# Optimization experiments

Measured on AMD Instinct MI355X. Metric: run time of the kernel, lower is better.

Reference implementation:

```python
import jax, jax.numpy as jnp
import numpy as np

N_QUBITS = 12
LAYERS = 4
ENCODERS = ['angle_rx', 'angle_ry', 'h_angle_rx', 'h_angle_ry']

_INV_SQRT2 = 1.0 / np.sqrt(2.0)
H_GATE = jnp.array([[_INV_SQRT2, _INV_SQRT2], [_INV_SQRT2, -_INV_SQRT2]], dtype=jnp.complex64)


def rx_mat(t):
    # t: scalar or (B,) -> (...,2,2)
    c = jnp.cos(t / 2).astype(jnp.complex64)
    s = jnp.sin(t / 2).astype(jnp.complex64)
    return jnp.stack([jnp.stack([c, -1j * s], -1), jnp.stack([-1j * s, c], -1)], -2)


def ry_mat(t):
    c = jnp.cos(t / 2).astype(jnp.complex64)
    s = jnp.sin(t / 2).astype(jnp.complex64)
    return jnp.stack([jnp.stack([c, -s], -1), jnp.stack([s, c], -1)], -2)


def rz_mat(t):
    e = jnp.exp(-1j * t.astype(jnp.complex64) / 2)
    z = jnp.zeros_like(e)
    return jnp.stack([jnp.stack([e, z], -1), jnp.stack([z, jnp.conj(e)], -1)], -2)


def apply_1q(state, U, q, n):
    # state: (B, 2^n); wire q is axis q in big-endian (PennyLane) ordering
    B = state.shape[0]
    L, R = 2 ** q, 2 ** (n - q - 1)
    s = state.reshape(B, L, 2, R)
    if U.ndim == 2:
        s = jnp.einsum('ab,BLbR->BLaR', U, s)
    else:  # per-sample gate (B,2,2)
        s = jnp.einsum('Bab,BLbR->BLaR', U, s)
    return s.reshape(B, 2 ** n)


def apply_cnot_adjacent(state, q, n):
    # CNOT(control=q, target=q+1)
    B = state.shape[0]
    L, R = 2 ** q, 2 ** (n - q - 2)
    s = state.reshape(B, L, 2, 2, R)
    s = jnp.stack([s[:, :, 0], s[:, :, 1, ::-1]], axis=2)
    return s.reshape(B, 2 ** n)


def run_circuit(features, theta, encoder, n, layers):
    B = features.shape[0]
    state = jnp.zeros((B, 2 ** n), dtype=jnp.complex64).at[:, 0].set(1.0)
    use_h = encoder.startswith('h_')
    rot = rx_mat if encoder.endswith('rx') else ry_mat
    # encoding: one angle per qubit, batched gate
    for q in range(n):
        if use_h:
            state = apply_1q(state, H_GATE, q, n)
        state = apply_1q(state, rot(features[:, q]), q, n)
    # variational block (hadamard=False)
    for l in range(layers):
        for q in range(n):
            state = apply_1q(state, rx_mat(theta[l, q, 0]), q, n)
            state = apply_1q(state, ry_mat(theta[l, q, 1]), q, n)
            state = apply_1q(state, rz_mat(theta[l, q, 2]), q, n)
        for q in range(0, n - 1, 2):
            state = apply_cnot_adjacent(state, q, n)
        for q in range(1, n - 1, 2):
            state = apply_cnot_adjacent(state, q, n)
    # <Z_q> for every qubit
    p = jnp.abs(state) ** 2  # (B, 2^n)
    ez = []
    for q in range(n):
        pr = p.reshape(B, 2 ** q, 2, -1)
        ez.append(pr[:, :, 0].sum((1, 2)) - pr[:, :, 1].sum((1, 2)))
    return jnp.stack(ez, axis=-1)  # (B, n)


def setup_inputs() -> dict:
    key = jax.random.key(0)
    k1, k2 = jax.random.split(key)
    features = jax.random.uniform(k1, (1024, N_QUBITS), dtype=jnp.float32)
    theta = 0.01 * jax.random.normal(k2, (LAYERS, N_QUBITS, 3), dtype=jnp.float32)
    alpha = jnp.zeros((len(ENCODERS),), dtype=jnp.float32)
    return {"features": features, "theta": theta, "alpha": alpha}


def reference(features, theta, alpha):
    arch_w = jax.nn.softmax(alpha)
    branch = jnp.stack(
        [run_circuit(features, theta, enc, N_QUBITS, LAYERS) for enc in ENCODERS], axis=0
    )  # (E, B, n_qubits)
    y = jnp.einsum('e,ebq->bq', arch_w, branch)
    return y
```

## Files before the change

kernel.cpp:

```cpp
#include <hip/hip_runtime.h>
#include <math.h>

#define NQ 12
#define DIM 4096
#define NL 4
#define THREADS 256
#define SWZC(e) ((e) ^ (((e) >> 3) & 14) ^ (((e) >> 7) & 15))
#define WAVEFENCE() { __builtin_amdgcn_wave_barrier(); __builtin_amdgcn_sched_barrier(0); }

typedef float v2f __attribute__((ext_vector_type(2)));

__device__ __forceinline__ v2f pkfma(v2f a, v2f b, v2f c) {
    v2f d; asm("v_pk_fma_f32 %0, %1, %2, %3" : "=v"(d) : "v"(a), "v"(b), "v"(c)); return d;
}
__device__ __forceinline__ v2f pkmul(v2f a, v2f b) {
    v2f d; asm("v_pk_mul_f32 %0, %1, %2" : "=v"(d) : "v"(a), "v"(b)); return d;
}
__device__ __forceinline__ v2f pkadd(v2f a, v2f b) {
    v2f d; asm("v_pk_add_f32 %0, %1, %2" : "=v"(d) : "v"(a), "v"(b)); return d;
}
__device__ __forceinline__ float2 cmulS(float2 a, float2 b) {
    return make_float2(fmaf(a.x, b.x, -a.y * b.y), fmaf(a.x, b.y, a.y * b.x));
}

struct C4 { v2f r, i, ni, nr; };

#define CMUL4(orE, orI, KR, KNI, KI, xre, xim) \
    { orE = pkfma(KNI, xim, pkmul(KR, xre)); orI = pkfma(KI, xre, pkmul(KR, xim)); }
#define CMAC4(orE, orI, KR, KNI, KI, xre, xim) \
    { orE = pkfma(KR, xre, pkfma(KNI, xim, orE)); orI = pkfma(KR, xim, pkfma(KI, xre, orI)); }

#define QUADBODY(A_, B_, C_, D_) { \
    v2f z0r,z0i,z1r,z1i,z2r,z2i,z3r,z3i; \
    CMUL4(z0r,z0i, la.r, la.ni, la.i, sre[A_], sim[A_]); CMAC4(z0r,z0i, lb.r, lb.ni, lb.i, sre[B_], sim[B_]); \
    CMUL4(z1r,z1i, lb.nr, lb.ni, lb.i, sre[A_], sim[A_]); CMAC4(z1r,z1i, la.r, la.i, la.ni, sre[B_], sim[B_]); \
    CMUL4(z2r,z2i, la.r, la.ni, la.i, sre[C_], sim[C_]); CMAC4(z2r,z2i, lb.r, lb.ni, lb.i, sre[D_], sim[D_]); \
    CMUL4(z3r,z3i, lb.nr, lb.ni, lb.i, sre[C_], sim[C_]); CMAC4(z3r,z3i, la.r, la.i, la.ni, sre[D_], sim[D_]); \
    v2f y0r,y0i,y1r,y1i,y2r,y2i,y3r,y3i; \
    CMUL4(y0r,y0i, ha.r, ha.ni, ha.i, z0r, z0i); CMAC4(y0r,y0i, hb.r, hb.ni, hb.i, z2r, z2i); \
    CMUL4(y1r,y1i, ha.r, ha.ni, ha.i, z1r, z1i); CMAC4(y1r,y1i, hb.r, hb.ni, hb.i, z3r, z3i); \
    CMUL4(y2r,y2i, hb.nr, hb.ni, hb.i, z0r, z0i); CMAC4(y2r,y2i, ha.r, ha.i, ha.ni, z2r, z2i); \
    CMUL4(y3r,y3i, hb.nr, hb.ni, hb.i, z1r, z1i); CMAC4(y3r,y3i, ha.r, ha.i, ha.ni, z3r, z3i); \
    sre[A_]=y0r; sim[A_]=y0i; sre[B_]=y1r; sim[B_]=y1i; \
    sre[C_]=y3r; sim[C_]=y3i; sre[D_]=y2r; sim[D_]=y2i; }

__device__ __forceinline__ void pass_hi(v2f* sre, v2f* sim, const v2f (*U)[4]) {
    C4 la={U[0][0],U[0][1],U[0][2],U[0][3]}, lb={U[1][0],U[1][1],U[1][2],U[1][3]},
       ha={U[2][0],U[2][1],U[2][2],U[2][3]}, hb={U[3][0],U[3][1],U[3][2],U[3][3]};
    QUADBODY(0,4,8,12) QUADBODY(1,5,9,13) QUADBODY(2,6,10,14) QUADBODY(3,7,11,15)
}
__device__ __forceinline__ void pass_lo(v2f* sre, v2f* sim, const v2f (*U)[4]) {
    C4 la={U[0][0],U[0][1],U[0][2],U[0][3]}, lb={U[1][0],U[1][1],U[1][2],U[1][3]},
       ha={U[2][0],U[2][1],U[2][2],U[2][3]}, hb={U[3][0],U[3][1],U[3][2],U[3][3]};
    QUADBODY(0,1,2,3) QUADBODY(4,5,6,7) QUADBODY(8,9,10,11) QUADBODY(12,13,14,15)
}

__global__ __launch_bounds__(THREADS, 2)
void vqc_kernel(const float* __restrict__ features,
                const float* __restrict__ theta,
                const float* __restrict__ alpha,
                float* __restrict__ out)
{
    __shared__ v2f scrR[DIM];
    __shared__ v2f scrI[DIM];
    __shared__ v2f Upk[24][4][4];
    __shared__ v2f red[12 * 4];
    __shared__ float wez[12];

    float2* cs = (float2*)scrR;
    float2 (*U48)[4] = (float2(*)[4])((char*)scrR + 1152);
    float2 (*enc)[2] = (float2(*)[2])((char*)scrR + 2688);
    float2 (*pairT)[4] = (float2(*)[4])((char*)scrR + 3072);
    float2* loc = (float2*)((char*)scrR + 3456);

    const int tid = threadIdx.x;
    const bool special = (blockIdx.x == 0);
    const int gA = special ? 0 : 2 * ((int)blockIdx.x - 1);
    const int gB = gA + 1;

    if (tid < NL * NQ * 3) {
        float s, c; sincosf(0.5f * theta[tid], &s, &c);
        cs[tid] = make_float2(c, s);
    }
    if (tid >= 160 && tid < 184) {
        int c_ = (tid - 160) / 12, q = (tid - 160) % 12;
        const float r_ = 0.70710678118654752f;
        float2 a0, a1;
        if (special) { a0 = make_float2(r_, 0.f); a1 = a0; }
        else {
            int g = c_ ? gB : gA;
            int esl = g % 3, b = g / 3;
            float f = features[b * NQ + q];
            float s, c; sincosf(0.5f * f, &s, &c);
            if (esl == 0)      { a0 = make_float2(c, 0.f); a1 = make_float2(0.f, -s); }
            else if (esl == 1) { a0 = make_float2(c, 0.f); a1 = make_float2(s, 0.f); }
            else               { a0 = make_float2((c-s)*r_, 0.f); a1 = make_float2((c+s)*r_, 0.f); }
        }
        enc[c_ * NQ + q][0] = a0; enc[c_ * NQ + q][1] = a1;
    }
    __syncthreads();

    if (tid < NL * NQ) {
        float c0 = cs[tid*3+0].x, s0 = cs[tid*3+0].y;
        float c1 = cs[tid*3+1].x, s1 = cs[tid*3+1].y;
        float c2 = cs[tid*3+2].x, s2 = cs[tid*3+2].y;
        float2 a00 = make_float2( c1*c0,  s1*s0);
        float2 a01 = make_float2(-s1*c0, -c1*s0);
        float2 a10 = make_float2( s1*c0, -c1*s0);
        float2 a11 = make_float2( c1*c0, -s1*s0);
        float2 ep = make_float2(c2, -s2), em = make_float2(c2, s2);
        U48[tid][0] = cmulS(ep, a00); U48[tid][1] = cmulS(ep, a01);
        U48[tid][2] = cmulS(em, a10); U48[tid][3] = cmulS(em, a11);
    }
    if (tid >= 64 && tid < 112) {
        int x = tid - 64;
        int c_ = x / 24, y = x % 24, p = y >> 2, v = y & 3;
        pairT[c_ * 6 + p][v] = cmulS(enc[c_*NQ + 2*p][v >> 1], enc[c_*NQ + 2*p + 1][v & 1]);
    }
    __syncthreads();

    for (int idx = tid; idx < 384; idx += THREADS) {
        int p = idx >> 4, rest = idx & 15, c = rest >> 2, comp = rest & 3;
        int l = p / 6, m = p % 6;
        int q = (c < 2) ? (2*m + 1) : (2*m);
        float2 u = U48[l*NQ + q][c & 1];
        float xv = (comp == 0) ? u.x : (comp == 1) ? u.y : (comp == 2) ? -u.y : -u.x;
        v2f vv = {xv, xv};
        Upk[p][c][comp] = vv;
    }
    if (tid >= 192 && tid < 224) {
        int x = tid - 192; int c_ = x >> 4, j = x & 15;
        loc[c_ * 16 + j] = cmulS(pairT[c_*6 + 4][j >> 2], pairT[c_*6 + 5][j & 3]);
    }
    __syncthreads();

    v2f sre[16], sim[16];
    {
        int t = tid;
        float2 preA = cmulS(cmulS(pairT[0][(t>>6)&3], pairT[1][(t>>4)&3]),
                            cmulS(pairT[2][(t>>2)&3], pairT[3][t&3]));
        float2 preB = cmulS(cmulS(pairT[6][(t>>6)&3], pairT[7][(t>>4)&3]),
                            cmulS(pairT[8][(t>>2)&3], pairT[9][t&3]));
        #pragma unroll
        for (int j = 0; j < 16; ++j) {
            float2 aA = cmulS(preA, loc[j]);
            float2 aB = cmulS(preB, loc[16 + j]);
            v2f r = {aA.x, aB.x}, ii = {aA.y, aB.y};
            sre[j] = r; sim[j] = ii;
        }
    }
    __syncthreads();

    const int ba = SWZC(tid << 4);
    const int bb = SWZC((((tid >> 4) << 8) | (tid & 15)));
    const int bc = SWZC(tid);
    const int sx = (tid << 4) ^ ((tid & 1) << 3) ^ (((tid >> 2) & 1) << 5)
                             ^ (((tid >> 4) & 1) << 7) ^ (((tid >> 6) & 1) << 9);
    const int bs = SWZC(sx);

    #pragma unroll 1
    for (int l = 0; l < NL; ++l) {
        if (l > 0) {
            #pragma unroll
            for (int j = 0; j < 16; ++j) {
                int a = bs ^ (j ^ ((j >> 1) & 2));
                sre[j] = scrR[a]; sim[j] = scrI[a];
            }
        }
        pass_hi(sre, sim, Upk[l*6 + 4]);
        pass_lo(sre, sim, Upk[l*6 + 5]);
        WAVEFENCE();
        #pragma unroll
        for (int j = 0; j < 16; ++j) { int a = ba ^ j; scrR[a] = sre[j]; scrI[a] = sim[j]; }
        WAVEFENCE();
        #pragma unroll
        for (int j = 0; j < 16; ++j) { int a = bb ^ SWZC(j << 4); sre[j] = scrR[a]; sim[j] = scrI[a]; }
        pass_hi(sre, sim, Upk[l*6 + 2]);
        pass_lo(sre, sim, Upk[l*6 + 3]);
        WAVEFENCE();
        #pragma unroll
        for (int j = 0; j < 16; ++j) { int a = bb ^ SWZC(j << 4); scrR[a] = sre[j]; scrI[a] = sim[j]; }
        __syncthreads();
        #pragma unroll
        for (int j = 0; j < 16; ++j) { int a = bc ^ SWZC(j << 8); sre[j] = scrR[a]; sim[j] = scrI[a]; }
        pass_hi(sre, sim, Upk[l*6 + 0]);
        if (l < NL - 1) __syncthreads();
        pass_lo(sre, sim, Upk[l*6 + 1]);
        if (l < NL - 1) {
            #pragma unroll
            for (int j = 0; j < 16; ++j) { int a = bc ^ SWZC(j << 8); scrR[a] = sre[j]; scrI[a] = sim[j]; }
            __syncthreads();
        }
    }

    v2f s0 = {0.f,0.f}, s1 = {0.f,0.f}, s2 = {0.f,0.f}, s3 = {0.f,0.f}, psum = {0.f,0.f};
    {
        const v2f MONE = {-1.f, -1.f};
        #pragma unroll
        for (int j = 0; j < 16; ++j) {
            v2f p = pkfma(sim[j], sim[j], pkmul(sre[j], sre[j]));
            psum = pkadd(psum, p);
            if (j & 8)                        s0 = pkfma(p, MONE, s0); else s0 = pkadd(s0, p);
            if (j & 4)                        s1 = pkfma(p, MONE, s1); else s1 = pkadd(s1, p);
            if ((((j >> 1) ^ (j >> 2)) & 1))  s2 = pkfma(p, MONE, s2); else s2 = pkadd(s2, p);
            if (j & 1)                        s3 = pkfma(p, MONE, s3); else s3 = pkadd(s3, p);
        }
    }
    v2f vals[12];
    {
        int t = tid;
        int mt = t ^ ((t >> 1) & 0xAA);
        vals[0] = s0; vals[1] = s1; vals[2] = s2; vals[3] = s3;
        vals[4]  = ((t >> 7) & 1)  ? -s3 : s3;
        vals[5]  = ((mt >> 6) & 1) ? -psum : psum;
        vals[6]  = ((mt >> 5) & 1) ? -psum : psum;
        vals[7]  = ((mt >> 4) & 1) ? -psum : psum;
        vals[8]  = ((mt >> 3) & 1) ? -psum : psum;
        vals[9]  = ((mt >> 2) & 1) ? -psum : psum;
        vals[10] = ((mt >> 1) & 1) ? -psum : psum;
        vals[11] = (mt & 1)        ? -psum : psum;
    }
    const int lane = tid & 63, wv = tid >> 6;
    #pragma unroll
    for (int q = 0; q < 12; ++q) {
        v2f v = vals[q];
        #pragma unroll
        for (int mm = 32; mm >= 1; mm >>= 1) {
            v.x += __shfl_xor(v.x, mm, 64);
            v.y += __shfl_xor(v.y, mm, 64);
        }
        if (lane == 0) red[q * 4 + wv] = v;
    }
    __syncthreads();

    if (tid < 12) {
        v2f v = pkadd(pkadd(red[tid*4+0], red[tid*4+1]), pkadd(red[tid*4+2], red[tid*4+3]));
        float A0 = alpha[0], A1 = alpha[1], A2 = alpha[2], A3 = alpha[3];
        float mx = fmaxf(fmaxf(A0, A1), fmaxf(A2, A3));
        float E0 = expf(A0-mx), E1 = expf(A1-mx), E2 = expf(A2-mx), E3 = expf(A3-mx);
        float den = E0 + E1 + E2 + E3;
        if (special) {
            wez[tid] = (E2 / den) * v.x;
        } else {
            int eslA = gA % 3, bA = gA / 3;
            int eslB = gB % 3, bB = gB / 3;
            float wA = ((eslA == 0) ? E0 : (eslA == 1) ? E1 : E3) / den;
            float wB = ((eslB == 0) ? E0 : (eslB == 1) ? E1 : E3) / den;
            atomicAdd(out + bA * NQ + tid, wA * v.x);
            atomicAdd(out + bB * NQ + tid, wB * v.y);
        }
    }
    if (special) {
        __syncthreads();
        for (int bb2 = tid; bb2 < 1024; bb2 += THREADS) {
            #pragma unroll
            for (int q = 0; q < NQ; ++q)
                atomicAdd(out + bb2 * NQ + q, wez[q]);
        }
    }
}

extern "C" void kernel_launch(void* const* d_in, const int* in_sizes, int n_in,
                              void* d_out, int out_size, void* d_ws, size_t ws_size,
                              hipStream_t stream) {
    const float* features = (const float*)d_in[0];
    const float* theta    = (const float*)d_in[1];
    const float* alpha    = (const float*)d_in[2];
    float* out = (float*)d_out;

    hipMemsetAsync(out, 0, (size_t)out_size * sizeof(float), stream);
    vqc_kernel<<<dim3(1537), THREADS, 0, stream>>>(features, theta, alpha, out);
}
```

Measured before the change: 139.4 us.

## Process four circuits per block with 128-bit LDS exchanges

```diff
diff --git a/kernel.cpp b/kernel.cpp
--- a/kernel.cpp
+++ b/kernel.cpp
@@ -9,6 +9,7 @@
 #define WAVEFENCE() { __builtin_amdgcn_wave_barrier(); __builtin_amdgcn_sched_barrier(0); }
 
 typedef float v2f __attribute__((ext_vector_type(2)));
+typedef float v4f __attribute__((ext_vector_type(4)));
 
 __device__ __forceinline__ v2f pkfma(v2f a, v2f b, v2f c) {
     v2f d; asm("v_pk_fma_f32 %0, %1, %2, %3" : "=v"(d) : "v"(a), "v"(b), "v"(c)); return d;
@@ -44,16 +45,23 @@
     sre[A_]=y0r; sim[A_]=y0i; sre[B_]=y1r; sim[B_]=y1i; \
     sre[C_]=y3r; sim[C_]=y3i; sre[D_]=y2r; sim[D_]=y2i; }
 
-__device__ __forceinline__ void pass_hi(v2f* sre, v2f* sim, const v2f (*U)[4]) {
+#define RUNQUADS_HI QUADBODY(0,4,8,12) QUADBODY(1,5,9,13) QUADBODY(2,6,10,14) QUADBODY(3,7,11,15)
+#define RUNQUADS_LO QUADBODY(0,1,2,3) QUADBODY(4,5,6,7) QUADBODY(8,9,10,11) QUADBODY(12,13,14,15)
+
+__device__ __forceinline__ void pass_hi2(v2f* r0, v2f* i0, v2f* r1, v2f* i1, const v2f (*U)[4]) {
     C4 la={U[0][0],U[0][1],U[0][2],U[0][3]}, lb={U[1][0],U[1][1],U[1][2],U[1][3]},
        ha={U[2][0],U[2][1],U[2][2],U[2][3]}, hb={U[3][0],U[3][1],U[3][2],U[3][3]};
-    QUADBODY(0,4,8,12) QUADBODY(1,5,9,13) QUADBODY(2,6,10,14) QUADBODY(3,7,11,15)
-}
-__device__ __forceinline__ void pass_lo(v2f* sre, v2f* sim, const v2f (*U)[4]) {
+    { v2f* sre=r0; v2f* sim=i0; RUNQUADS_HI }
+    { v2f* sre=r1; v2f* sim=i1; RUNQUADS_HI }
+}
+__device__ __forceinline__ void pass_lo2(v2f* r0, v2f* i0, v2f* r1, v2f* i1, const v2f (*U)[4]) {
     C4 la={U[0][0],U[0][1],U[0][2],U[0][3]}, lb={U[1][0],U[1][1],U[1][2],U[1][3]},
        ha={U[2][0],U[2][1],U[2][2],U[2][3]}, hb={U[3][0],U[3][1],U[3][2],U[3][3]};
-    QUADBODY(0,1,2,3) QUADBODY(4,5,6,7) QUADBODY(8,9,10,11) QUADBODY(12,13,14,15)
-}
+    { v2f* sre=r0; v2f* sim=i0; RUNQUADS_LO }
+    { v2f* sre=r1; v2f* sim=i1; RUNQUADS_LO }
+}
+
+__device__ __forceinline__ v4f pack4(v2f a, v2f b) { v4f t; t[0]=a[0]; t[1]=a[1]; t[2]=b[0]; t[3]=b[1]; return t; }
 
 __global__ __launch_bounds__(THREADS, 2)
 void vqc_kernel(const float* __restrict__ features,
@@ -61,34 +69,32 @@
                 const float* __restrict__ alpha,
                 float* __restrict__ out)
 {
-    __shared__ v2f scrR[DIM];
-    __shared__ v2f scrI[DIM];
+    __shared__ v4f scr4[DIM];
     __shared__ v2f Upk[24][4][4];
-    __shared__ v2f red[12 * 4];
+    __shared__ v4f red[12 * 4];
     __shared__ float wez[12];
 
-    float2* cs = (float2*)scrR;
-    float2 (*U48)[4] = (float2(*)[4])((char*)scrR + 1152);
-    float2 (*enc)[2] = (float2(*)[2])((char*)scrR + 2688);
-    float2 (*pairT)[4] = (float2(*)[4])((char*)scrR + 3072);
-    float2* loc = (float2*)((char*)scrR + 3456);
+    float2* cs = (float2*)scr4;
+    float2 (*U48)[4] = (float2(*)[4])((char*)scr4 + 1152);
+    float2 (*enc)[2] = (float2(*)[2])((char*)scr4 + 2688);
+    float2 (*pairT)[4] = (float2(*)[4])((char*)scr4 + 3456);
+    float2* loc = (float2*)((char*)scr4 + 4224);
 
     const int tid = threadIdx.x;
     const bool special = (blockIdx.x == 0);
-    const int gA = special ? 0 : 2 * ((int)blockIdx.x - 1);
-    const int gB = gA + 1;
+    const int gBase = special ? 0 : 4 * ((int)blockIdx.x - 1);
 
     if (tid < NL * NQ * 3) {
         float s, c; sincosf(0.5f * theta[tid], &s, &c);
         cs[tid] = make_float2(c, s);
     }
-    if (tid >= 160 && tid < 184) {
+    if (tid >= 160 && tid < 208) {
         int c_ = (tid - 160) / 12, q = (tid - 160) % 12;
         const float r_ = 0.70710678118654752f;
         float2 a0, a1;
         if (special) { a0 = make_float2(r_, 0.f); a1 = a0; }
         else {
-            int g = c_ ? gB : gA;
+            int g = gBase + c_;
             int esl = g % 3, b = g / 3;
             float f = features[b * NQ + q];
             float s, c; sincosf(0.5f * f, &s, &c);
@@ -112,7 +118,7 @@
         U48[tid][0] = cmulS(ep, a00); U48[tid][1] = cmulS(ep, a01);
         U48[tid][2] = cmulS(em, a10); U48[tid][3] = cmulS(em, a11);
     }
-    if (tid >= 64 && tid < 112) {
+    if (tid >= 64 && tid < 160) {
         int x = tid - 64;
         int c_ = x / 24, y = x % 24, p = y >> 2, v = y & 3;
         pairT[c_ * 6 + p][v] = cmulS(enc[c_*NQ + 2*p][v >> 1], enc[c_*NQ + 2*p + 1][v & 1]);
@@ -128,25 +134,29 @@
         v2f vv = {xv, xv};
         Upk[p][c][comp] = vv;
     }
-    if (tid >= 192 && tid < 224) {
+    if (tid >= 192 && tid < 256) {
         int x = tid - 192; int c_ = x >> 4, j = x & 15;
         loc[c_ * 16 + j] = cmulS(pairT[c_*6 + 4][j >> 2], pairT[c_*6 + 5][j & 3]);
     }
     __syncthreads();
 
-    v2f sre[16], sim[16];
+    v2f r0[16], i0[16], r1[16], i1[16];
     {
         int t = tid;
-        float2 preA = cmulS(cmulS(pairT[0][(t>>6)&3], pairT[1][(t>>4)&3]),
-                            cmulS(pairT[2][(t>>2)&3], pairT[3][t&3]));
-        float2 preB = cmulS(cmulS(pairT[6][(t>>6)&3], pairT[7][(t>>4)&3]),
-                            cmulS(pairT[8][(t>>2)&3], pairT[9][t&3]));
+        float2 pre[4];
+        #pragma unroll
+        for (int c = 0; c < 4; ++c)
+            pre[c] = cmulS(cmulS(pairT[c*6+0][(t>>6)&3], pairT[c*6+1][(t>>4)&3]),
+                           cmulS(pairT[c*6+2][(t>>2)&3], pairT[c*6+3][t&3]));
         #pragma unroll
         for (int j = 0; j < 16; ++j) {
-            float2 aA = cmulS(preA, loc[j]);
-            float2 aB = cmulS(preB, loc[16 + j]);
-            v2f r = {aA.x, aB.x}, ii = {aA.y, aB.y};
-            sre[j] = r; sim[j] = ii;
+            float2 aA = cmulS(pre[0], loc[j]);
+            float2 aB = cmulS(pre[1], loc[16 + j]);
+            float2 aC = cmulS(pre[2], loc[32 + j]);
+            float2 aD = cmulS(pre[3], loc[48 + j]);
+            v2f ra = {aA.x, aB.x}; v2f ia = {aA.y, aB.y};
+            v2f rb = {aC.x, aD.x}; v2f ib = {aC.y, aD.y};
+            r0[j] = ra; i0[j] = ia; r1[j] = rb; i1[j] = ib;
         }
     }
     __syncthreads();
@@ -160,94 +170,113 @@
 
     #pragma unroll 1
     for (int l = 0; l < NL; ++l) {
-        if (l > 0) {
-            #pragma unroll
-            for (int j = 0; j < 16; ++j) {
-                int a = bs ^ (j ^ ((j >> 1) & 2));
-                sre[j] = scrR[a]; sim[j] = scrI[a];
-            }
-        }
-        pass_hi(sre, sim, Upk[l*6 + 4]);
-        pass_lo(sre, sim, Upk[l*6 + 5]);
-        WAVEFENCE();
-        #pragma unroll
-        for (int j = 0; j < 16; ++j) { int a = ba ^ j; scrR[a] = sre[j]; scrI[a] = sim[j]; }
-        WAVEFENCE();
-        #pragma unroll
-        for (int j = 0; j < 16; ++j) { int a = bb ^ SWZC(j << 4); sre[j] = scrR[a]; sim[j] = scrI[a]; }
-        pass_hi(sre, sim, Upk[l*6 + 2]);
-        pass_lo(sre, sim, Upk[l*6 + 3]);
-        WAVEFENCE();
-        #pragma unroll
-        for (int j = 0; j < 16; ++j) { int a = bb ^ SWZC(j << 4); scrR[a] = sre[j]; scrI[a] = sim[j]; }
-        __syncthreads();
-        #pragma unroll
-        for (int j = 0; j < 16; ++j) { int a = bc ^ SWZC(j << 8); sre[j] = scrR[a]; sim[j] = scrI[a]; }
-        pass_hi(sre, sim, Upk[l*6 + 0]);
-        if (l < NL - 1) __syncthreads();
-        pass_lo(sre, sim, Upk[l*6 + 1]);
+        pass_hi2(r0, i0, r1, i1, Upk[l*6 + 4]);
+        pass_lo2(r0, i0, r1, i1, Upk[l*6 + 5]);
+        WAVEFENCE();
+        #pragma unroll
+        for (int j = 0; j < 16; ++j) scr4[ba ^ j] = pack4(r0[j], r1[j]);
+        WAVEFENCE();
+        #pragma unroll
+        for (int j = 0; j < 16; ++j) { v4f t = scr4[bb ^ SWZC(j << 4)]; v2f a={t[0],t[1]}, b={t[2],t[3]}; r0[j]=a; r1[j]=b; }
+        WAVEFENCE();
+        #pragma unroll
+        for (int j = 0; j < 16; ++j) scr4[ba ^ j] = pack4(i0[j], i1[j]);
+        WAVEFENCE();
+        #pragma unroll
+        for (int j = 0; j < 16; ++j) { v4f t = scr4[bb ^ SWZC(j << 4)]; v2f a={t[0],t[1]}, b={t[2],t[3]}; i0[j]=a; i1[j]=b; }
+        WAVEFENCE();
+        pass_hi2(r0, i0, r1, i1, Upk[l*6 + 2]);
+        pass_lo2(r0, i0, r1, i1, Upk[l*6 + 3]);
+        WAVEFENCE();
+        #pragma unroll
+        for (int j = 0; j < 16; ++j) scr4[bb ^ SWZC(j << 4)] = pack4(r0[j], r1[j]);
+        __syncthreads();
+        #pragma unroll
+        for (int j = 0; j < 16; ++j) { v4f t = scr4[bc ^ SWZC(j << 8)]; v2f a={t[0],t[1]}, b={t[2],t[3]}; r0[j]=a; r1[j]=b; }
+        __syncthreads();
+        #pragma unroll
+        for (int j = 0; j < 16; ++j) scr4[bb ^ SWZC(j << 4)] = pack4(i0[j], i1[j]);
+        __syncthreads();
+        #pragma unroll
+        for (int j = 0; j < 16; ++j) { v4f t = scr4[bc ^ SWZC(j << 8)]; v2f a={t[0],t[1]}, b={t[2],t[3]}; i0[j]=a; i1[j]=b; }
+        pass_hi2(r0, i0, r1, i1, Upk[l*6 + 0]);
+        __syncthreads();
+        pass_lo2(r0, i0, r1, i1, Upk[l*6 + 1]);
         if (l < NL - 1) {
             #pragma unroll
-            for (int j = 0; j < 16; ++j) { int a = bc ^ SWZC(j << 8); scrR[a] = sre[j]; scrI[a] = sim[j]; }
+            for (int j = 0; j < 16; ++j) scr4[bc ^ SWZC(j << 8)] = pack4(r0[j], r1[j]);
             __syncthreads();
-        }
-    }
-
-    v2f s0 = {0.f,0.f}, s1 = {0.f,0.f}, s2 = {0.f,0.f}, s3 = {0.f,0.f}, psum = {0.f,0.f};
+            #pragma unroll
+            for (int j = 0; j < 16; ++j) { int a_ = bs ^ (j ^ ((j >> 1) & 2)); v4f t = scr4[a_]; v2f a={t[0],t[1]}, b={t[2],t[3]}; r0[j]=a; r1[j]=b; }
+            __syncthreads();
+            #pragma unroll
+            for (int j = 0; j < 16; ++j) scr4[bc ^ SWZC(j << 8)] = pack4(i0[j], i1[j]);
+            __syncthreads();
+            #pragma unroll
+            for (int j = 0; j < 16; ++j) { int a_ = bs ^ (j ^ ((j >> 1) & 2)); v4f t = scr4[a_]; v2f a={t[0],t[1]}, b={t[2],t[3]}; i0[j]=a; i1[j]=b; }
+            WAVEFENCE();
+        }
+    }
+
+    v2f s0a={0,0}, s1a={0,0}, s2a={0,0}, s3a={0,0}, pa={0,0};
+    v2f s0b={0,0}, s1b={0,0}, s2b={0,0}, s3b={0,0}, pb={0,0};
     {
         const v2f MONE = {-1.f, -1.f};
         #pragma unroll
         for (int j = 0; j < 16; ++j) {
-            v2f p = pkfma(sim[j], sim[j], pkmul(sre[j], sre[j]));
-            psum = pkadd(psum, p);
-            if (j & 8)                        s0 = pkfma(p, MONE, s0); else s0 = pkadd(s0, p);
-            if (j & 4)                        s1 = pkfma(p, MONE, s1); else s1 = pkadd(s1, p);
-            if ((((j >> 1) ^ (j >> 2)) & 1))  s2 = pkfma(p, MONE, s2); else s2 = pkadd(s2, p);
-            if (j & 1)                        s3 = pkfma(p, MONE, s3); else s3 = pkadd(s3, p);
-        }
-    }
-    v2f vals[12];
+            v2f p0 = pkfma(i0[j], i0[j], pkmul(r0[j], r0[j]));
+            v2f p1 = pkfma(i1[j], i1[j], pkmul(r1[j], r1[j]));
+            pa = pkadd(pa, p0); pb = pkadd(pb, p1);
+            if (j & 8) { s0a = pkfma(p0, MONE, s0a); s0b = pkfma(p1, MONE, s0b); } else { s0a = pkadd(s0a, p0); s0b = pkadd(s0b, p1); }
+            if (j & 4) { s1a = pkfma(p0, MONE, s1a); s1b = pkfma(p1, MONE, s1b); } else { s1a = pkadd(s1a, p0); s1b = pkadd(s1b, p1); }
+            if ((((j >> 1) ^ (j >> 2)) & 1)) { s2a = pkfma(p0, MONE, s2a); s2b = pkfma(p1, MONE, s2b); } else { s2a = pkadd(s2a, p0); s2b = pkadd(s2b, p1); }
+            if (j & 1) { s3a = pkfma(p0, MONE, s3a); s3b = pkfma(p1, MONE, s3b); } else { s3a = pkadd(s3a, p0); s3b = pkadd(s3b, p1); }
+        }
+    }
+    v2f va[12], vb[12];
     {
         int t = tid;
         int mt = t ^ ((t >> 1) & 0xAA);
-        vals[0] = s0; vals[1] = s1; vals[2] = s2; vals[3] = s3;
-        vals[4]  = ((t >> 7) & 1)  ? -s3 : s3;
-        vals[5]  = ((mt >> 6) & 1) ? -psum : psum;
-        vals[6]  = ((mt >> 5) & 1) ? -psum : psum;
-        vals[7]  = ((mt >> 4) & 1) ? -psum : psum;
-        vals[8]  = ((mt >> 3) & 1) ? -psum : psum;
-        vals[9]  = ((mt >> 2) & 1) ? -psum : psum;
-        vals[10] = ((mt >> 1) & 1) ? -psum : psum;
-        vals[11] = (mt & 1)        ? -psum : psum;
+        va[0]=s0a; va[1]=s1a; va[2]=s2a; va[3]=s3a;
+        vb[0]=s0b; vb[1]=s1b; vb[2]=s2b; vb[3]=s3b;
+        va[4] = ((t >> 7) & 1) ? -s3a : s3a;  vb[4] = ((t >> 7) & 1) ? -s3b : s3b;
+        #pragma unroll
+        for (int q = 5; q < 12; ++q) {
+            int bit = (mt >> (11 - q)) & 1;
+            va[q] = bit ? -pa : pa;  vb[q] = bit ? -pb : pb;
+        }
     }
     const int lane = tid & 63, wv = tid >> 6;
     #pragma unroll
     for (int q = 0; q < 12; ++q) {
-        v2f v = vals[q];
+        v4f v = pack4(va[q], vb[q]);
         #pragma unroll
         for (int mm = 32; mm >= 1; mm >>= 1) {
-            v.x += __shfl_xor(v.x, mm, 64);
-            v.y += __shfl_xor(v.y, mm, 64);
+            v[0] += __shfl_xor(v[0], mm, 64);
+            v[1] += __shfl_xor(v[1], mm, 64);
+            v[2] += __shfl_xor(v[2], mm, 64);
+            v[3] += __shfl_xor(v[3], mm, 64);
         }
         if (lane == 0) red[q * 4 + wv] = v;
     }
     __syncthreads();
 
     if (tid < 12) {
-        v2f v = pkadd(pkadd(red[tid*4+0], red[tid*4+1]), pkadd(red[tid*4+2], red[tid*4+3]));
+        v4f v = red[tid*4+0] + red[tid*4+1] + red[tid*4+2] + red[tid*4+3];
         float A0 = alpha[0], A1 = alpha[1], A2 = alpha[2], A3 = alpha[3];
         float mx = fmaxf(fmaxf(A0, A1), fmaxf(A2, A3));
         float E0 = expf(A0-mx), E1 = expf(A1-mx), E2 = expf(A2-mx), E3 = expf(A3-mx);
         float den = E0 + E1 + E2 + E3;
         if (special) {
-            wez[tid] = (E2 / den) * v.x;
+            wez[tid] = (E2 / den) * v[0];
         } else {
-            int eslA = gA % 3, bA = gA / 3;
-            int eslB = gB % 3, bB = gB / 3;
-            float wA = ((eslA == 0) ? E0 : (eslA == 1) ? E1 : E3) / den;
-            float wB = ((eslB == 0) ? E0 : (eslB == 1) ? E1 : E3) / den;
-            atomicAdd(out + bA * NQ + tid, wA * v.x);
-            atomicAdd(out + bB * NQ + tid, wB * v.y);
+            #pragma unroll
+            for (int c = 0; c < 4; ++c) {
+                int g = gBase + c;
+                int esl = g % 3, b = g / 3;
+                float w = ((esl == 0) ? E0 : (esl == 1) ? E1 : E3) / den;
+                atomicAdd(out + b * NQ + tid, w * v[c]);
+            }
         }
     }
     if (special) {
@@ -269,5 +298,5 @@
     float* out = (float*)d_out;
 
     hipMemsetAsync(out, 0, (size_t)out_size * sizeof(float), stream);
-    vqc_kernel<<<dim3(1537), THREADS, 0, stream>>>(features, theta, alpha, out);
-}
+    vqc_kernel<<<dim3(769), THREADS, 0, stream>>>(features, theta, alpha, out);
+}
```

After: 149.9 us. +7.6%, slower.

## Interleave real/imag state in v4f LDS layout and unify per-layer pass loop

Applied to the files above, without the earlier changes.

```diff
diff --git a/kernel.cpp b/kernel.cpp
--- a/kernel.cpp
+++ b/kernel.cpp
@@ -5,10 +5,9 @@
 #define DIM 4096
 #define NL 4
 #define THREADS 256
-#define SWZC(e) ((e) ^ (((e) >> 3) & 14) ^ (((e) >> 7) & 15))
-#define WAVEFENCE() { __builtin_amdgcn_wave_barrier(); __builtin_amdgcn_sched_barrier(0); }
 
 typedef float v2f __attribute__((ext_vector_type(2)));
+typedef float v4f __attribute__((ext_vector_type(4)));
 
 __device__ __forceinline__ v2f pkfma(v2f a, v2f b, v2f c) {
     v2f d; asm("v_pk_fma_f32 %0, %1, %2, %3" : "=v"(d) : "v"(a), "v"(b), "v"(c)); return d;
@@ -22,6 +21,9 @@
 __device__ __forceinline__ float2 cmulS(float2 a, float2 b) {
     return make_float2(fmaf(a.x, b.x, -a.y * b.y), fmaf(a.x, b.y, a.y * b.x));
 }
+
+__device__ __forceinline__ int sigp(int i) { return i ^ ((i >> 1) & 0x2AA); }
+__device__ __forceinline__ int swz(int i) { return i ^ ((i >> 3) & 7) ^ ((i >> 6) & 7) ^ ((i >> 9) & 7); }
 
 struct C4 { v2f r, i, ni, nr; };
 
@@ -55,23 +57,23 @@
     QUADBODY(0,1,2,3) QUADBODY(4,5,6,7) QUADBODY(8,9,10,11) QUADBODY(12,13,14,15)
 }
 
+__device__ __forceinline__ v4f pack4(v2f a, v2f b) { v4f t; t[0]=a[0]; t[1]=a[1]; t[2]=b[0]; t[3]=b[1]; return t; }
+
 __global__ __launch_bounds__(THREADS, 2)
 void vqc_kernel(const float* __restrict__ features,
                 const float* __restrict__ theta,
                 const float* __restrict__ alpha,
                 float* __restrict__ out)
 {
-    __shared__ v2f scrR[DIM];
-    __shared__ v2f scrI[DIM];
+    __shared__ v4f st[DIM];
+    __shared__ float2 cs[NL * NQ * 3];
+    __shared__ float2 U48[NL * NQ][4];
+    __shared__ float2 enc[2 * NQ][2];
+    __shared__ float2 pairT[12][4];
+    __shared__ float2 loc[32];
     __shared__ v2f Upk[24][4][4];
     __shared__ v2f red[12 * 4];
     __shared__ float wez[12];
-
-    float2* cs = (float2*)scrR;
-    float2 (*U48)[4] = (float2(*)[4])((char*)scrR + 1152);
-    float2 (*enc)[2] = (float2(*)[2])((char*)scrR + 2688);
-    float2 (*pairT)[4] = (float2(*)[4])((char*)scrR + 3072);
-    float2* loc = (float2*)((char*)scrR + 3456);
 
     const int tid = threadIdx.x;
     const bool special = (blockIdx.x == 0);
@@ -149,47 +151,39 @@
             sre[j] = r; sim[j] = ii;
         }
     }
-    __syncthreads();
-
-    const int ba = SWZC(tid << 4);
-    const int bb = SWZC((((tid >> 4) << 8) | (tid & 15)));
-    const int bc = SWZC(tid);
-    const int sx = (tid << 4) ^ ((tid & 1) << 3) ^ (((tid >> 2) & 1) << 5)
-                             ^ (((tid >> 4) & 1) << 7) ^ (((tid >> 6) & 1) << 9);
-    const int bs = SWZC(sx);
-
-    #pragma unroll 1
+
+    const int baseA = tid << 4;
+    const int baseB = ((tid & 0xF0) << 4) | (tid & 15);
+    const int baseC = tid;
+    const int AB0[3] = { swz(baseA), swz(baseB), swz(baseC) };
+    const int AB1[3] = { swz(sigp(baseA)), swz(sigp(baseB)), swz(sigp(baseC)) };
+
+    #pragma unroll
     for (int l = 0; l < NL; ++l) {
-        if (l > 0) {
+        const int par = l & 1;
+        #pragma unroll
+        for (int w = 0; w < 3; ++w) {
+            const int S = 4 * w;
+            const int hx = l*6 + (4 - 2*w);
+            int addr[16];
             #pragma unroll
-            for (int j = 0; j < 16; ++j) {
-                int a = bs ^ (j ^ ((j >> 1) & 2));
-                sre[j] = scrR[a]; sim[j] = scrI[a];
+            for (int jj = 0; jj < 16; ++jj) {
+                const int j = ((jj & 3) << 2) | (jj >> 2);
+                const int cj = par ? swz(sigp(j << S)) : swz(j << S);
+                addr[j] = (par ? AB1[w] : AB0[w]) ^ cj;
+                if (!(l == 0 && w == 0)) {
+                    v4f t = st[addr[j]];
+                    v2f r = {t[0], t[1]}, ii = {t[2], t[3]};
+                    sre[j] = r; sim[j] = ii;
+                }
             }
-        }
-        pass_hi(sre, sim, Upk[l*6 + 4]);
-        pass_lo(sre, sim, Upk[l*6 + 5]);
-        WAVEFENCE();
-        #pragma unroll
-        for (int j = 0; j < 16; ++j) { int a = ba ^ j; scrR[a] = sre[j]; scrI[a] = sim[j]; }
-        WAVEFENCE();
-        #pragma unroll
-        for (int j = 0; j < 16; ++j) { int a = bb ^ SWZC(j << 4); sre[j] = scrR[a]; sim[j] = scrI[a]; }
-        pass_hi(sre, sim, Upk[l*6 + 2]);
-        pass_lo(sre, sim, Upk[l*6 + 3]);
-        WAVEFENCE();
-        #pragma unroll
-        for (int j = 0; j < 16; ++j) { int a = bb ^ SWZC(j << 4); scrR[a] = sre[j]; scrI[a] = sim[j]; }
-        __syncthreads();
-        #pragma unroll
-        for (int j = 0; j < 16; ++j) { int a = bc ^ SWZC(j << 8); sre[j] = scrR[a]; sim[j] = scrI[a]; }
-        pass_hi(sre, sim, Upk[l*6 + 0]);
-        if (l < NL - 1) __syncthreads();
-        pass_lo(sre, sim, Upk[l*6 + 1]);
-        if (l < NL - 1) {
-            #pragma unroll
-            for (int j = 0; j < 16; ++j) { int a = bc ^ SWZC(j << 8); scrR[a] = sre[j]; scrI[a] = sim[j]; }
-            __syncthreads();
+            pass_hi(sre, sim, Upk[hx]);
+            pass_lo(sre, sim, Upk[hx + 1]);
+            if (!(l == NL-1 && w == 2)) {
+                #pragma unroll
+                for (int j = 0; j < 16; ++j) st[addr[j]] = pack4(sre[j], sim[j]);
+                __syncthreads();
+            }
         }
     }
 
```

Measured after the change: 140.6 us. About the same (+0.9%).

## Store LDS statevector scratch as packed fp16 to halve shared memory

Applied to the files above, without the earlier changes.

```diff
diff --git a/kernel.cpp b/kernel.cpp
--- a/kernel.cpp
+++ b/kernel.cpp
@@ -1,4 +1,5 @@
 #include <hip/hip_runtime.h>
+#include <hip/hip_fp16.h>
 #include <math.h>
 
 #define NQ 12
@@ -21,6 +22,21 @@
 }
 __device__ __forceinline__ float2 cmulS(float2 a, float2 b) {
     return make_float2(fmaf(a.x, b.x, -a.y * b.y), fmaf(a.x, b.y, a.y * b.x));
+}
+
+__device__ __forceinline__ uint2 packh(v2f re, v2f im) {
+    __half2 a = __floats2half2_rn(re[0], re[1]);
+    __half2 b = __floats2half2_rn(im[0], im[1]);
+    uint2 r;
+    r.x = __builtin_bit_cast(unsigned int, a);
+    r.y = __builtin_bit_cast(unsigned int, b);
+    return r;
+}
+__device__ __forceinline__ void unpackh(uint2 t, v2f* re, v2f* im) {
+    float2 fa = __half22float2(__builtin_bit_cast(__half2, t.x));
+    float2 fb = __half22float2(__builtin_bit_cast(__half2, t.y));
+    v2f r = {fa.x, fa.y}, i = {fb.x, fb.y};
+    *re = r; *im = i;
 }
 
 struct C4 { v2f r, i, ni, nr; };
@@ -55,23 +71,22 @@
     QUADBODY(0,1,2,3) QUADBODY(4,5,6,7) QUADBODY(8,9,10,11) QUADBODY(12,13,14,15)
 }
 
-__global__ __launch_bounds__(THREADS, 2)
+__global__ __attribute__((amdgpu_flat_work_group_size(256, 256), amdgpu_waves_per_eu(2, 8)))
 void vqc_kernel(const float* __restrict__ features,
                 const float* __restrict__ theta,
                 const float* __restrict__ alpha,
                 float* __restrict__ out)
 {
-    __shared__ v2f scrR[DIM];
-    __shared__ v2f scrI[DIM];
+    __shared__ uint2 scrH[DIM];
     __shared__ v2f Upk[24][4][4];
     __shared__ v2f red[12 * 4];
     __shared__ float wez[12];
 
-    float2* cs = (float2*)scrR;
-    float2 (*U48)[4] = (float2(*)[4])((char*)scrR + 1152);
-    float2 (*enc)[2] = (float2(*)[2])((char*)scrR + 2688);
-    float2 (*pairT)[4] = (float2(*)[4])((char*)scrR + 3072);
-    float2* loc = (float2*)((char*)scrR + 3456);
+    float2* cs = (float2*)scrH;
+    float2 (*U48)[4] = (float2(*)[4])((char*)scrH + 1152);
+    float2 (*enc)[2] = (float2(*)[2])((char*)scrH + 2688);
+    float2 (*pairT)[4] = (float2(*)[4])((char*)scrH + 3072);
+    float2* loc = (float2*)((char*)scrH + 3456);
 
     const int tid = threadIdx.x;
     const bool special = (blockIdx.x == 0);
@@ -164,31 +179,32 @@
             #pragma unroll
             for (int j = 0; j < 16; ++j) {
                 int a = bs ^ (j ^ ((j >> 1) & 2));
-                sre[j] = scrR[a]; sim[j] = scrI[a];
+                unpackh(scrH[a], &sre[j], &sim[j]);
             }
+            __syncthreads();
         }
         pass_hi(sre, sim, Upk[l*6 + 4]);
         pass_lo(sre, sim, Upk[l*6 + 5]);
         WAVEFENCE();
         #pragma unroll
-        for (int j = 0; j < 16; ++j) { int a = ba ^ j; scrR[a] = sre[j]; scrI[a] = sim[j]; }
+        for (int j = 0; j < 16; ++j) scrH[ba ^ j] = packh(sre[j], sim[j]);
         WAVEFENCE();
         #pragma unroll
-        for (int j = 0; j < 16; ++j) { int a = bb ^ SWZC(j << 4); sre[j] = scrR[a]; sim[j] = scrI[a]; }
+        for (int j = 0; j < 16; ++j) unpackh(scrH[bb ^ SWZC(j << 4)], &sre[j], &sim[j]);
         pass_hi(sre, sim, Upk[l*6 + 2]);
         pass_lo(sre, sim, Upk[l*6 + 3]);
         WAVEFENCE();
         #pragma unroll
-        for (int j = 0; j < 16; ++j) { int a = bb ^ SWZC(j << 4); scrR[a] = sre[j]; scrI[a] = sim[j]; }
+        for (int j = 0; j < 16; ++j) scrH[bb ^ SWZC(j << 4)] = packh(sre[j], sim[j]);
         __syncthreads();
         #pragma unroll
-        for (int j = 0; j < 16; ++j) { int a = bc ^ SWZC(j << 8); sre[j] = scrR[a]; sim[j] = scrI[a]; }
+        for (int j = 0; j < 16; ++j) unpackh(scrH[bc ^ SWZC(j << 8)], &sre[j], &sim[j]);
         pass_hi(sre, sim, Upk[l*6 + 0]);
-        if (l < NL - 1) __syncthreads();
         pass_lo(sre, sim, Upk[l*6 + 1]);
         if (l < NL - 1) {
+            WAVEFENCE();
             #pragma unroll
-            for (int j = 0; j < 16; ++j) { int a = bc ^ SWZC(j << 8); scrR[a] = sre[j]; scrI[a] = sim[j]; }
+            for (int j = 0; j < 16; ++j) scrH[bc ^ SWZC(j << 8)] = packh(sre[j], sim[j]);
             __syncthreads();
         }
     }
```

Result: faster. 125.5 us (-9.9%).
